# Kernel optimization log

Measured on AMD Instinct MI355X. Metric: run time of the kernel, lower is better.

The kernel has to match this reference:

```python
import jax, jax.numpy as jnp
import numpy as np

EPS = 1e-12


def _l2norm(x, axis):
    return x / jnp.maximum(jnp.linalg.norm(x, axis=axis, keepdims=True), EPS)


def _wn_weight(v, g):
    # weight norm over input axis (kernel_size=1): W = g * v / ||v||
    return g * v / jnp.maximum(jnp.linalg.norm(v, axis=0, keepdims=True), EPS)


def setup_inputs() -> dict:
    key = jax.random.key(0)
    ks = jax.random.split(key, 8)
    B, T, D = 16, 4096, 512
    N, K, d = 9, 1024, 8
    return {
        "z": jax.random.normal(ks[0], (B, T, D), dtype=jnp.float32),
        "in_v": jax.random.normal(ks[1], (N, D, d), dtype=jnp.float32) * 0.05,
        "in_g": jax.random.uniform(ks[2], (N, d), dtype=jnp.float32) + 0.5,
        "in_b": jax.random.normal(ks[3], (N, d), dtype=jnp.float32) * 0.01,
        "out_v": jax.random.normal(ks[4], (N, d, D), dtype=jnp.float32) * 0.05,
        "out_g": jax.random.uniform(ks[5], (N, D), dtype=jnp.float32) + 0.5,
        "out_b": jax.random.normal(ks[6], (N, D), dtype=jnp.float32) * 0.01,
        "codebooks": jax.random.normal(ks[7], (N, K, d), dtype=jnp.float32),
    }


def reference(z, in_v, in_g, in_b, out_v, out_g, out_b, codebooks):
    # Eval-mode ResidualVectorQuantize: n_quantizers = n_codebooks, mask all True.
    n_codebooks = codebooks.shape[0]
    residual = z
    z_q = jnp.zeros_like(z)
    commitment_loss = jnp.zeros((), z.dtype)
    codebook_loss = jnp.zeros((), z.dtype)
    codes, latents = [], []
    for i in range(n_codebooks):
        # in_proj (weight-normalized 1x1 conv == linear): [B,T,D] -> [B,T,d]
        W_in = _wn_weight(in_v[i], in_g[i])
        z_e = jnp.einsum("btd,dc->btc", residual, W_in) + in_b[i]
        # decode_latents: l2-normalize, pairwise sq-dist, nearest neighbor
        cb = codebooks[i]                      # [K, d] raw codebook
        enc_n = _l2norm(z_e, axis=-1)          # [B, T, d]
        cb_n = _l2norm(cb, axis=-1)            # [K, d]
        dist = (jnp.sum(enc_n * enc_n, -1, keepdims=True)
                - 2.0 * jnp.einsum("btc,kc->btk", enc_n, cb_n)
                + jnp.sum(cb_n * cb_n, -1))    # [B, T, K]
        indices = jnp.argmax(-dist, axis=-1)   # [B, T]
        z_q_i = cb[indices]                    # gather from raw codebook [B,T,d]
        # per-batch losses (mean over T, d)
        commit_i = jnp.mean((z_e - jax.lax.stop_gradient(z_q_i)) ** 2, axis=(1, 2))
        cbloss_i = jnp.mean((z_q_i - jax.lax.stop_gradient(z_e)) ** 2, axis=(1, 2))
        # straight-through estimator
        z_q_st = z_e + jax.lax.stop_gradient(z_q_i - z_e)
        # out_proj: [B,T,d] -> [B,T,D]
        W_out = _wn_weight(out_v[i], out_g[i])
        z_q_proj = jnp.einsum("btc,cd->btd", z_q_st, W_out) + out_b[i]
        z_q = z_q + z_q_proj
        residual = residual - z_q_proj
        commitment_loss = commitment_loss + commit_i.mean()
        codebook_loss = codebook_loss + cbloss_i.mean()
        codes.append(indices)
        latents.append(z_e)
    codes = jnp.stack(codes, axis=2)           # [B, T, N]
    latents = jnp.concatenate(latents, axis=2) # [B, T, N*d]
    return z_q, codes, latents, commitment_loss, codebook_loss
```

## Files before the change

kernel.cpp:

```cpp
#include <hip/hip_runtime.h>
#include <math.h>

#define ROWS   65536

#define WS_WPAD 0
#define WS_WOUT 49152
#define WS_CBT  86016
#define WS_SC   159744
#define WS_M    168960
#define WS_CACC 174144
#define WS_SOB  174216
#define WS_LOSS 174728

#define OUT_CODES 33554432
#define OUT_LAT   34144256
#define OUT_CLOSS 38862848
#define OUT_CBLOSS 38862849

#define SM_AST   0
#define SM_BS    4224
#define SM_P     0
#define SM_QLT   0
#define SM_REG2  9216
#define SM_CODES 18720
#define SM_WARR  19872

typedef float v2f __attribute__((ext_vector_type(2)));
__device__ __forceinline__ v2f fma2(v2f a, v2f b, v2f c){
    return __builtin_elementwise_fma(a, b, c);
}

__device__ __forceinline__ int pcol(int cc){ return (cc/9)*12 + (cc%9); }

__global__ __launch_bounds__(256) void prep1(const float* __restrict__ in_v,
    const float* __restrict__ in_g, const float* __restrict__ out_v,
    const float* __restrict__ out_g, const float* __restrict__ out_b,
    const float* __restrict__ cb, float* __restrict__ ws)
{
    int t = blockIdx.x*256 + threadIdx.x;
    if (t < 9216) {
        int i = t >> 10, k = t & 1023;
        const float* p = cb + (i*1024 + k)*8;
        float v[8]; float ssq = 0.f;
        #pragma unroll
        for (int c=0;c<8;c++){ v[c]=p[c]; ssq = fmaf(v[c],v[c],ssq); }
        float den = fmaxf(sqrtf(ssq), 1e-12f);
        float sc = 0.f;
        #pragma unroll
        for (int c=0;c<8;c++){ float cn = v[c]/den; ws[WS_CBT + (i*8+c)*1024 + k] = cn; sc = fmaf(cn,cn,sc); }
        ws[WS_SC + i*1024 + k] = sc;
    } else if (t < 13824) {
        int r = t - 9216; int j = r >> 9, tt = r & 511;
        float v[8]; float ssq = 0.f;
        #pragma unroll
        for (int a=0;a<8;a++){ v[a]=out_v[(j*8+a)*512+tt]; ssq=fmaf(v[a],v[a],ssq); }
        float den = fmaxf(sqrtf(ssq), 1e-12f);
        float g = out_g[j*512+tt];
        #pragma unroll
        for (int a=0;a<8;a++) ws[WS_WOUT + (j*8+a)*512 + tt] = g*v[a]/den;
    } else if (t < 18432) {
        int r = t - 13824;
        int w = r >> 6, l = r & 63;
        int i = w >> 3, c = w & 7;
        float v[8]; float ssq = 0.f;
        #pragma unroll
        for (int u=0;u<8;u++){ v[u] = in_v[(i*512 + l*8+u)*8 + c]; ssq = fmaf(v[u],v[u],ssq); }
        #pragma unroll
        for (int off=1; off<64; off<<=1) ssq += __shfl_xor(ssq, off, 64);
        float den = fmaxf(sqrtf(ssq), 1e-12f);
        float g = in_g[i*8+c];
        int pc = pcol(i*8+c);
        #pragma unroll
        for (int u=0;u<8;u++) ws[WS_WPAD + (l*8+u)*96 + pc] = g*v[u]/den;
    } else if (t < 18944) {
        int tt = t - 18432;
        float s = 0.f;
        for (int j=0;j<9;j++) s += out_b[j*512+tt];
        ws[WS_SOB + tt] = s;
    } else if (t == 18944) {
        *(double*)&ws[WS_LOSS] = 0.0;
    }
}

__global__ __launch_bounds__(256) void prep2(const float* __restrict__ out_b,
                                             float* __restrict__ ws)
{
    int g = blockIdx.x*256 + threadIdx.x;
    if (g < 41472) {
        int oi = g >> 3, part = g & 7;
        int j = oi / 576; int rem = oi % 576; int i = rem >> 6; int ab = rem & 63;
        int a = ab >> 3, b = ab & 7;
        int pc = pcol(i*8+b);
        const float* wo = ws + WS_WOUT + (j*8+a)*512 + part*64;
        const float* wp = ws + WS_WPAD + (part*64)*96 + pc;
        float s = 0.f;
        #pragma unroll
        for (int u=0; u<16; u++) {
            float4 w4 = *(const float4*)(wo + u*4);
            s = fmaf(w4.x, wp[(u*4+0)*96], s);
            s = fmaf(w4.y, wp[(u*4+1)*96], s);
            s = fmaf(w4.z, wp[(u*4+2)*96], s);
            s = fmaf(w4.w, wp[(u*4+3)*96], s);
        }
        #pragma unroll
        for (int off=1; off<8; off<<=1) s += __shfl_xor(s, off, 64);
        if (part == 0) ws[WS_M + oi] = s;
    } else if (g < 42048) {
        int r = g - 41472;
        int oi = r >> 3, part = r & 7;
        int i = oi >> 3, b = oi & 7;
        int pc = pcol(i*8+b);
        float s = 0.f;
        for (int u=0; u<64; u++) {
            int tt = part*64 + u;
            float bb = 0.f;
            for (int j=0;j<i;j++) bb += out_b[j*512+tt];
            s = fmaf(bb, ws[WS_WPAD + tt*96+pc], s);
        }
        #pragma unroll
        for (int off=1; off<8; off<<=1) s += __shfl_xor(s, off, 64);
        if (part == 0) ws[WS_CACC + oi] = s;
    }
}

__global__ __launch_bounds__(256, 2) void fused_all(
    const float* __restrict__ z, const float* __restrict__ in_b,
    const float* __restrict__ cbooks, float* __restrict__ ws, float* __restrict__ out)
{
    __shared__ __align__(16) float smem[19880];
    int tid = threadIdx.x;
    int brow = blockIdx.x * 128;

    {
        float* AsT = smem + SM_AST;
        float* Bs  = smem + SM_BS;
        int tr = tid & 31, tc = tid >> 5;
        v2f accp[4][4]; float acc8[4];
        #pragma unroll
        for (int r=0;r<4;r++){
            #pragma unroll
            for(int t2=0;t2<4;t2++) accp[r][t2] = (v2f){0.f,0.f};
            acc8[r]=0.f;
        }
        int kq = tid & 7, rr = tid >> 3;
        for (int kk=0; kk<16; kk++) {
            #pragma unroll
            for (int p=0;p<4;p++){
                int row = rr + p*32;
                float4 a = *(const float4*)(z + (size_t)(brow+row)*512 + kk*32 + kq*4);
                AsT[(kq     )*132 + row] = a.x;
                AsT[(kq +  8)*132 + row] = a.y;
                AsT[(kq + 16)*132 + row] = a.z;
                AsT[(kq + 24)*132 + row] = a.w;
            }
            #pragma unroll
            for (int p=0;p<3;p++){
                int idx = p*256 + tid;
                *(float4*)(Bs + idx*4) = *(const float4*)(ws + WS_WPAD + kk*32*96 + idx*4);
            }
            __syncthreads();
            #pragma unroll 4
            for (int k=0;k<32;k++){
                int sk = ((k&3)<<3) | (k>>2);
                float4 a  = *(const float4*)(AsT + sk*132 + tr*4);
                float4 b0 = *(const float4*)(Bs + k*96 + tc*12);
                float4 b1 = *(const float4*)(Bs + k*96 + tc*12 + 4);
                float  b8 = Bs[k*96 + tc*12 + 8];
                float av[4] = {a.x,a.y,a.z,a.w};
                v2f bp[4] = {{b0.x,b0.y},{b0.z,b0.w},{b1.x,b1.y},{b1.z,b1.w}};
                #pragma unroll
                for (int r=0;r<4;r++){
                    v2f ar = {av[r], av[r]};
                    #pragma unroll
                    for (int t2=0;t2<4;t2++) accp[r][t2] = fma2(ar, bp[t2], accp[r][t2]);
                    acc8[r] = fmaf(av[r], b8, acc8[r]);
                }
            }
            __syncthreads();
        }
        float* P = smem + SM_P;
        #pragma unroll
        for (int c=0;c<9;c++){
            int cc = tc*9+c;
            float bias = in_b[cc];
            #pragma unroll
            for (int r=0;r<4;r++){
                int rl = tr*4 + r;
                float val = (c<8) ? accp[r][c>>1][c&1] : acc8[r];
                P[rl*72 + cc] = val + bias;
            }
        }
        __syncthreads();
    }

    int w  = tid >> 6;
    int l  = tid & 63;
    int rowhalf = l >> 1;
    int ah = l & 1;
    int wrow = brow + w*32;
    int kb = l*16;
    float* P = smem + SM_P;
    float* zen_w = smem + SM_REG2 + w*384;
    float* codes_lds = smem + SM_CODES;

    float lacc = 0.f;
    v2f cbp[8][8];
    v2f hp[8];

    #pragma unroll 1
    for (int i=0; i<9; i++){
        const float* cbb = ws + WS_CBT + i*8192 + kb;
        #pragma unroll
        for (int c=0;c<8;c++){
            float4 A0 = *(const float4*)(cbb + c*1024);
            float4 A1 = *(const float4*)(cbb + c*1024 + 4);
            float4 A2 = *(const float4*)(cbb + c*1024 + 8);
            float4 A3 = *(const float4*)(cbb + c*1024 + 12);
            cbp[0][c] = (v2f){A0.x,A0.y}; cbp[1][c] = (v2f){A0.z,A0.w};
            cbp[2][c] = (v2f){A1.x,A1.y}; cbp[3][c] = (v2f){A1.z,A1.w};
            cbp[4][c] = (v2f){A2.x,A2.y}; cbp[5][c] = (v2f){A2.z,A2.w};
            cbp[6][c] = (v2f){A3.x,A3.y}; cbp[7][c] = (v2f){A3.z,A3.w};
        }
        {
            const float* scb = ws + WS_SC + i*1024 + kb;
            float4 s0 = *(const float4*)(scb);
            float4 s1 = *(const float4*)(scb + 4);
            float4 s2 = *(const float4*)(scb + 8);
            float4 s3 = *(const float4*)(scb + 12);
            hp[0] = (v2f){s0.x*-0.5f, s0.y*-0.5f}; hp[1] = (v2f){s0.z*-0.5f, s0.w*-0.5f};
            hp[2] = (v2f){s1.x*-0.5f, s1.y*-0.5f}; hp[3] = (v2f){s1.z*-0.5f, s1.w*-0.5f};
            hp[4] = (v2f){s2.x*-0.5f, s2.y*-0.5f}; hp[5] = (v2f){s2.z*-0.5f, s2.w*-0.5f};
            hp[6] = (v2f){s3.x*-0.5f, s3.y*-0.5f}; hp[7] = (v2f){s3.z*-0.5f, s3.w*-0.5f};
        }

        int row = wrow + rowhalf;
        int rib = w*32 + rowhalf;
        float* lat = out + OUT_LAT + (size_t)row*72 + i*8;
        float4 p0 = *(const float4*)(P + rib*72 + i*8);
        float4 p1 = *(const float4*)(P + rib*72 + i*8 + 4);
        v2f zep[4] = {{p0.x,p0.y},{p0.z,p0.w},{p1.x,p1.y},{p1.z,p1.w}};
        #pragma unroll
        for (int t2=0;t2<4;t2++){
            v2f cp = {ws[WS_CACC + i*8 + 2*t2], ws[WS_CACC + i*8 + 2*t2+1]};
            zep[t2] -= cp;
        }
        #pragma unroll 1
        for (int j=0;j<i;j++){
            int kj = (int)codes_lds[rib*9 + j];
            const float* qp = cbooks + (size_t)(j*1024+kj)*8;
            float4 q0 = *(const float4*)(qp);
            float4 q1 = *(const float4*)(qp+4);
            float qa[8] = {q0.x,q0.y,q0.z,q0.w,q1.x,q1.y,q1.z,q1.w};
            const float* M = ws + WS_M + (j*9+i)*64;
            #pragma unroll
            for (int a=0;a<8;a++){
                float4 m0 = *(const float4*)(M + a*8);
                float4 m1 = *(const float4*)(M + a*8 + 4);
                v2f nqa = {-qa[a], -qa[a]};
                zep[0] = fma2(nqa, (v2f){m0.x,m0.y}, zep[0]);
                zep[1] = fma2(nqa, (v2f){m0.z,m0.w}, zep[1]);
                zep[2] = fma2(nqa, (v2f){m1.x,m1.y}, zep[2]);
                zep[3] = fma2(nqa, (v2f){m1.z,m1.w}, zep[3]);
            }
        }
        float ssq = 0.f;
        #pragma unroll
        for (int c=0;c<8;c++){ float zc = zep[c>>1][c&1]; ssq = fmaf(zc,zc,ssq); }
        float den = fmaxf(sqrtf(ssq), 1e-12f);
        float rden = 1.0f/den;
        v2f rd2 = {rden, rden};
        v2f zenp[4];
        #pragma unroll
        for (int t2=0;t2<4;t2++) zenp[t2] = zep[t2]*rd2;
        if (ah == 0){
            float4 n0 = {zenp[0][0],zenp[0][1],zenp[1][0],zenp[1][1]};
            float4 n1 = {zenp[2][0],zenp[2][1],zenp[3][0],zenp[3][1]};
            *(float4*)(zen_w + rowhalf*12)     = n0;
            *(float4*)(zen_w + rowhalf*12 + 4) = n1;
        } else {
            float4 z0 = {zep[0][0],zep[0][1],zep[1][0],zep[1][1]};
            float4 z1 = {zep[2][0],zep[2][1],zep[3][0],zep[3][1]};
            *(float4*)(lat)   = z0;
            *(float4*)(lat+4) = z1;
        }

        int ksave = 0;
        #pragma unroll 2
        for (int rr=0; rr<32; rr++){
            float4 zv0 = *(const float4*)(zen_w + rr*12);
            float4 zv1 = *(const float4*)(zen_w + rr*12 + 4);
            float zr[8] = {zv0.x,zv0.y,zv0.z,zv0.w,zv1.x,zv1.y,zv1.z,zv1.w};
            v2f dp[8];
            #pragma unroll
            for (int p=0;p<8;p++) dp[p] = hp[p];
            #pragma unroll
            for (int c=0;c<8;c++){
                v2f zc = {zr[c], zr[c]};
                #pragma unroll
                for (int p=0;p<8;p++) dp[p] = fma2(zc, cbp[p][c], dp[p]);
            }
            float bv = -3.0e38f; int rel = 0;
            #pragma unroll
            for (int p=0;p<8;p++){
                float de = dp[p][0];
                bool ce = de > bv; rel = ce ? (2*p)   : rel; bv = ce ? de : bv;
                float dohalf = dp[p][1];
                bool co = dohalf > bv; rel = co ? (2*p+1) : rel; bv = co ? dohalf : bv;
            }
            int kfull = kb + rel;
            float wm = bv;
            #pragma unroll
            for (int off=1; off<64; off<<=1) wm = fmaxf(wm, __shfl_xor(wm, off, 64));
            unsigned long long msk = __ballot(bv == wm);
            int ln = __ffsll((long long)msk) - 1;
            int kwin = __shfl(kfull, ln, 64);
            ksave = (rowhalf == rr) ? kwin : ksave;
        }

        if (ah == 0){
            const float* qp = cbooks + (size_t)(i*1024+ksave)*8;
            float4 q0 = *(const float4*)(qp);
            float4 q1 = *(const float4*)(qp+4);
            float e0 = zep[0][0]-q0.x, e1 = zep[0][1]-q0.y, e2 = zep[1][0]-q0.z, e3 = zep[1][1]-q0.w;
            float e4 = zep[2][0]-q1.x, e5 = zep[2][1]-q1.y, e6 = zep[3][0]-q1.z, e7 = zep[3][1]-q1.w;
            lacc = fmaf(e0,e0,lacc); lacc = fmaf(e1,e1,lacc);
            lacc = fmaf(e2,e2,lacc); lacc = fmaf(e3,e3,lacc);
            lacc = fmaf(e4,e4,lacc); lacc = fmaf(e5,e5,lacc);
            lacc = fmaf(e6,e6,lacc); lacc = fmaf(e7,e7,lacc);
        } else {
            out[OUT_CODES + (size_t)row*9 + i] = (float)ksave;
            codes_lds[rib*9 + i] = (float)ksave;
        }
    }

    {
        float* warr = smem + SM_WARR;
        #pragma unroll
        for (int off=1; off<64; off<<=1) lacc += __shfl_xor(lacc, off, 64);
        if ((tid & 63)==0) warr[w] = lacc;
        __syncthreads();
        if (tid==0){
            double bs = (double)warr[0]+(double)warr[1]+(double)warr[2]+(double)warr[3];
            atomicAdd((double*)&ws[WS_LOSS], bs);
        }
    }

    __syncthreads();
    {
        float* QLT = smem + SM_QLT;
        float* Ws  = smem + SM_REG2;
        if (tid < 128){
            for (int j=0;j<9;j++){
                int kj = (int)codes_lds[tid*9 + j];
                const float* qp = cbooks + (size_t)(j*1024+kj)*8;
                float4 q0 = *(const float4*)qp;
                float4 q1 = *(const float4*)(qp+4);
                QLT[(j*8+0)*128 + tid] = q0.x;
                QLT[(j*8+1)*128 + tid] = q0.y;
                QLT[(j*8+2)*128 + tid] = q0.z;
                QLT[(j*8+3)*128 + tid] = q0.w;
                QLT[(j*8+4)*128 + tid] = q1.x;
                QLT[(j*8+5)*128 + tid] = q1.y;
                QLT[(j*8+6)*128 + tid] = q1.z;
                QLT[(j*8+7)*128 + tid] = q1.w;
            }
        }
        int tc = tid & 15, tr = tid >> 4;
        int aoff = tr*8;
        int boff = tc*8 + (tc>>3)*4;
        for (int cc=0; cc<4; cc++){
            __syncthreads();
            #pragma unroll
            for (int p=0;p<9;p++){
                int idx = p*256 + tid;
                int jr = idx >> 5; int cq = idx & 31;
                float4 wv = *(const float4*)(ws + WS_WOUT + jr*512 + cc*128 + cq*4);
                *(float4*)(Ws + jr*132 + cq*4 + (cq>>4)*4) = wv;
            }
            __syncthreads();
            v2f accp[8][4];
            #pragma unroll
            for (int r=0;r<8;r++){
                #pragma unroll
                for (int t2=0;t2<4;t2++) accp[r][t2] = (v2f){0.f,0.f};
            }
            #pragma unroll 2
            for (int k=0;k<72;k++){
                float4 a0 = *(const float4*)(QLT + k*128 + aoff);
                float4 a1 = *(const float4*)(QLT + k*128 + aoff + 4);
                float4 b0 = *(const float4*)(Ws + k*132 + boff);
                float4 b1 = *(const float4*)(Ws + k*132 + boff + 4);
                float av[8] = {a0.x,a0.y,a0.z,a0.w,a1.x,a1.y,a1.z,a1.w};
                v2f wp[4] = {{b0.x,b0.y},{b0.z,b0.w},{b1.x,b1.y},{b1.z,b1.w}};
                #pragma unroll
                for (int r=0;r<8;r++){
                    v2f ar = {av[r], av[r]};
                    #pragma unroll
                    for (int t2=0;t2<4;t2++) accp[r][t2] = fma2(ar, wp[t2], accp[r][t2]);
                }
            }
            float4 s0 = *(const float4*)(ws + WS_SOB + cc*128 + tc*8);
            float4 s1 = *(const float4*)(ws + WS_SOB + cc*128 + tc*8 + 4);
            #pragma unroll
            for (int r=0;r<8;r++){
                int row = brow + tr*8 + r;
                float4 o0 = {accp[r][0][0]+s0.x, accp[r][0][1]+s0.y, accp[r][1][0]+s0.z, accp[r][1][1]+s0.w};
                float4 o1 = {accp[r][2][0]+s1.x, accp[r][2][1]+s1.y, accp[r][3][0]+s1.z, accp[r][3][1]+s1.w};
                *(float4*)(out + (size_t)row*512 + cc*128 + tc*8)     = o0;
                *(float4*)(out + (size_t)row*512 + cc*128 + tc*8 + 4) = o1;
            }
        }
    }
}

__global__ void finalize(const float* __restrict__ ws, float* __restrict__ out)
{
    if (threadIdx.x == 0){
        double L = *(const double*)(ws + WS_LOSS);
        float lv = (float)(L * (1.0/524288.0));
        out[OUT_CLOSS]  = lv;
        out[OUT_CBLOSS] = lv;
    }
}

extern "C" void kernel_launch(void* const* d_in, const int* in_sizes, int n_in,
                              void* d_out, int out_size, void* d_ws, size_t ws_size,
                              hipStream_t stream) {
    const float* z     = (const float*)d_in[0];
    const float* in_v  = (const float*)d_in[1];
    const float* in_g  = (const float*)d_in[2];
    const float* in_b  = (const float*)d_in[3];
    const float* out_v = (const float*)d_in[4];
    const float* out_g = (const float*)d_in[5];
    const float* out_b = (const float*)d_in[6];
    const float* cb    = (const float*)d_in[7];
    float* out = (float*)d_out;
    float* ws  = (float*)d_ws;

    prep1<<<75, 256, 0, stream>>>(in_v, in_g, out_v, out_g, out_b, cb, ws);
    prep2<<<165, 256, 0, stream>>>(out_b, ws);
    fused_all<<<512, 256, 0, stream>>>(z, in_b, cb, ws, out);
    finalize<<<1, 64, 0, stream>>>(ws, out);
}
```

Baseline: 585.5 us.

## Stream codebook halves per row pair to cut register pressure in argmax loop

The codebook slice (8x16 values) and scaled norms are no longer held in registers for the whole 32-row scan. Each row pair now reloads two 8-column halves from global/L2 and evaluates both rows against them. The per-lane argmax uses a tree reduction, the two rows' wave reductions are interleaved, and the loss work is split across both lane halves. The aim is to lower VGPR use for better occupancy and more ILP, at the cost of repeated codebook loads inside the row loop.

```diff
diff --git a/kernel.cpp b/kernel.cpp
--- a/kernel.cpp
+++ b/kernel.cpp
@@ -204,35 +204,9 @@
     float* codes_lds = smem + SM_CODES;
 
     float lacc = 0.f;
-    v2f cbp[8][8];
-    v2f hp[8];
 
     #pragma unroll 1
     for (int i=0; i<9; i++){
-        const float* cbb = ws + WS_CBT + i*8192 + kb;
-        #pragma unroll
-        for (int c=0;c<8;c++){
-            float4 A0 = *(const float4*)(cbb + c*1024);
-            float4 A1 = *(const float4*)(cbb + c*1024 + 4);
-            float4 A2 = *(const float4*)(cbb + c*1024 + 8);
-            float4 A3 = *(const float4*)(cbb + c*1024 + 12);
-            cbp[0][c] = (v2f){A0.x,A0.y}; cbp[1][c] = (v2f){A0.z,A0.w};
-            cbp[2][c] = (v2f){A1.x,A1.y}; cbp[3][c] = (v2f){A1.z,A1.w};
-            cbp[4][c] = (v2f){A2.x,A2.y}; cbp[5][c] = (v2f){A2.z,A2.w};
-            cbp[6][c] = (v2f){A3.x,A3.y}; cbp[7][c] = (v2f){A3.z,A3.w};
-        }
-        {
-            const float* scb = ws + WS_SC + i*1024 + kb;
-            float4 s0 = *(const float4*)(scb);
-            float4 s1 = *(const float4*)(scb + 4);
-            float4 s2 = *(const float4*)(scb + 8);
-            float4 s3 = *(const float4*)(scb + 12);
-            hp[0] = (v2f){s0.x*-0.5f, s0.y*-0.5f}; hp[1] = (v2f){s0.z*-0.5f, s0.w*-0.5f};
-            hp[2] = (v2f){s1.x*-0.5f, s1.y*-0.5f}; hp[3] = (v2f){s1.z*-0.5f, s1.w*-0.5f};
-            hp[4] = (v2f){s2.x*-0.5f, s2.y*-0.5f}; hp[5] = (v2f){s2.z*-0.5f, s2.w*-0.5f};
-            hp[6] = (v2f){s3.x*-0.5f, s3.y*-0.5f}; hp[7] = (v2f){s3.z*-0.5f, s3.w*-0.5f};
-        }
-
         int row = wrow + rowhalf;
         int rib = w*32 + rowhalf;
         float* lat = out + OUT_LAT + (size_t)row*72 + i*8;
@@ -241,8 +215,8 @@
         v2f zep[4] = {{p0.x,p0.y},{p0.z,p0.w},{p1.x,p1.y},{p1.z,p1.w}};
         #pragma unroll
         for (int t2=0;t2<4;t2++){
-            v2f cp = {ws[WS_CACC + i*8 + 2*t2], ws[WS_CACC + i*8 + 2*t2+1]};
-            zep[t2] -= cp;
+            v2f cp2 = {ws[WS_CACC + i*8 + 2*t2], ws[WS_CACC + i*8 + 2*t2+1]};
+            zep[t2] -= cp2;
         }
         #pragma unroll 1
         for (int j=0;j<i;j++){
@@ -269,12 +243,10 @@
         float den = fmaxf(sqrtf(ssq), 1e-12f);
         float rden = 1.0f/den;
         v2f rd2 = {rden, rden};
-        v2f zenp[4];
-        #pragma unroll
-        for (int t2=0;t2<4;t2++) zenp[t2] = zep[t2]*rd2;
         if (ah == 0){
-            float4 n0 = {zenp[0][0],zenp[0][1],zenp[1][0],zenp[1][1]};
-            float4 n1 = {zenp[2][0],zenp[2][1],zenp[3][0],zenp[3][1]};
+            v2f zn0 = zep[0]*rd2, zn1 = zep[1]*rd2, zn2 = zep[2]*rd2, zn3 = zep[3]*rd2;
+            float4 n0 = {zn0[0],zn0[1],zn1[0],zn1[1]};
+            float4 n1 = {zn2[0],zn2[1],zn3[0],zn3[1]};
             *(float4*)(zen_w + rowhalf*12)     = n0;
             *(float4*)(zen_w + rowhalf*12 + 4) = n1;
         } else {
@@ -283,53 +255,108 @@
             *(float4*)(lat)   = z0;
             *(float4*)(lat+4) = z1;
         }
+        v2f zh0 = ah ? zep[2] : zep[0];
+        v2f zh1 = ah ? zep[3] : zep[1];
 
         int ksave = 0;
-        #pragma unroll 2
-        for (int rr=0; rr<32; rr++){
-            float4 zv0 = *(const float4*)(zen_w + rr*12);
-            float4 zv1 = *(const float4*)(zen_w + rr*12 + 4);
-            float zr[8] = {zv0.x,zv0.y,zv0.z,zv0.w,zv1.x,zv1.y,zv1.z,zv1.w};
-            v2f dp[8];
-            #pragma unroll
-            for (int p=0;p<8;p++) dp[p] = hp[p];
-            #pragma unroll
-            for (int c=0;c<8;c++){
-                v2f zc = {zr[c], zr[c]};
+        #pragma unroll 1
+        for (int rr=0; rr<32; rr+=2){
+            const float* zA = zen_w + rr*12;
+            const float* zB = zen_w + rr*12 + 12;
+            float bvA = -3.0e38f, bvB = -3.0e38f; int relA = 0, relB = 0;
+            #pragma unroll 1
+            for (int h=0; h<2; h++){
+                const float* cbb = ws + WS_CBT + i*8192 + kb + h*8;
+                v2f cp[4][8];
                 #pragma unroll
-                for (int p=0;p<8;p++) dp[p] = fma2(zc, cbp[p][c], dp[p]);
-            }
-            float bv = -3.0e38f; int rel = 0;
-            #pragma unroll
-            for (int p=0;p<8;p++){
-                float de = dp[p][0];
-                bool ce = de > bv; rel = ce ? (2*p)   : rel; bv = ce ? de : bv;
-                float dohalf = dp[p][1];
-                bool co = dohalf > bv; rel = co ? (2*p+1) : rel; bv = co ? dohalf : bv;
-            }
-            int kfull = kb + rel;
-            float wm = bv;
-            #pragma unroll
-            for (int off=1; off<64; off<<=1) wm = fmaxf(wm, __shfl_xor(wm, off, 64));
-            unsigned long long msk = __ballot(bv == wm);
-            int ln = __ffsll((long long)msk) - 1;
-            int kwin = __shfl(kfull, ln, 64);
-            ksave = (rowhalf == rr) ? kwin : ksave;
-        }
-
-        if (ah == 0){
-            const float* qp = cbooks + (size_t)(i*1024+ksave)*8;
-            float4 q0 = *(const float4*)(qp);
-            float4 q1 = *(const float4*)(qp+4);
-            float e0 = zep[0][0]-q0.x, e1 = zep[0][1]-q0.y, e2 = zep[1][0]-q0.z, e3 = zep[1][1]-q0.w;
-            float e4 = zep[2][0]-q1.x, e5 = zep[2][1]-q1.y, e6 = zep[3][0]-q1.z, e7 = zep[3][1]-q1.w;
+                for (int c=0;c<8;c++){
+                    float4 A0 = *(const float4*)(cbb + c*1024);
+                    float4 A1 = *(const float4*)(cbb + c*1024 + 4);
+                    cp[0][c]=(v2f){A0.x,A0.y}; cp[1][c]=(v2f){A0.z,A0.w};
+                    cp[2][c]=(v2f){A1.x,A1.y}; cp[3][c]=(v2f){A1.z,A1.w};
+                }
+                const float* scb = ws + WS_SC + i*1024 + kb + h*8;
+                float4 s0 = *(const float4*)(scb);
+                float4 s1 = *(const float4*)(scb+4);
+                v2f hh[4] = {{s0.x*-0.5f,s0.y*-0.5f},{s0.z*-0.5f,s0.w*-0.5f},
+                             {s1.x*-0.5f,s1.y*-0.5f},{s1.z*-0.5f,s1.w*-0.5f}};
+                {
+                    float4 zv0 = *(const float4*)(zA);
+                    float4 zv1 = *(const float4*)(zA+4);
+                    float zr[8] = {zv0.x,zv0.y,zv0.z,zv0.w,zv1.x,zv1.y,zv1.z,zv1.w};
+                    v2f d[4] = {hh[0],hh[1],hh[2],hh[3]};
+                    #pragma unroll
+                    for (int c=0;c<8;c++){
+                        v2f zc = {zr[c], zr[c]};
+                        #pragma unroll
+                        for (int p=0;p<4;p++) d[p] = fma2(zc, cp[p][c], d[p]);
+                    }
+                    bool t;
+                    float va = d[0][0]; int ia = 0;
+                    t = d[0][1] > va; va = t?d[0][1]:va; ia = t?1:ia;
+                    float vb = d[1][0]; int ib = 2;
+                    t = d[1][1] > vb; vb = t?d[1][1]:vb; ib = t?3:ib;
+                    float vc = d[2][0]; int ic = 4;
+                    t = d[2][1] > vc; vc = t?d[2][1]:vc; ic = t?5:ic;
+                    float vd = d[3][0]; int id_ = 6;
+                    t = d[3][1] > vd; vd = t?d[3][1]:vd; id_ = t?7:id_;
+                    t = vb > va; va = t?vb:va; ia = t?ib:ia;
+                    t = vd > vc; vc = t?vd:vc; ic = t?id_:ic;
+                    t = vc > va; va = t?vc:va; ia = t?ic:ia;
+                    t = va > bvA; bvA = t?va:bvA; relA = t?(h*8+ia):relA;
+                }
+                {
+                    float4 zv0 = *(const float4*)(zB);
+                    float4 zv1 = *(const float4*)(zB+4);
+                    float zr[8] = {zv0.x,zv0.y,zv0.z,zv0.w,zv1.x,zv1.y,zv1.z,zv1.w};
+                    v2f d[4] = {hh[0],hh[1],hh[2],hh[3]};
+                    #pragma unroll
+                    for (int c=0;c<8;c++){
+                        v2f zc = {zr[c], zr[c]};
+                        #pragma unroll
+                        for (int p=0;p<4;p++) d[p] = fma2(zc, cp[p][c], d[p]);
+                    }
+                    bool t;
+                    float va = d[0][0]; int ia = 0;
+                    t = d[0][1] > va; va = t?d[0][1]:va; ia = t?1:ia;
+                    float vb = d[1][0]; int ib = 2;
+                    t = d[1][1] > vb; vb = t?d[1][1]:vb; ib = t?3:ib;
+                    float vc = d[2][0]; int ic = 4;
+                    t = d[2][1] > vc; vc = t?d[2][1]:vc; ic = t?5:ic;
+                    float vd = d[3][0]; int id_ = 6;
+                    t = d[3][1] > vd; vd = t?d[3][1]:vd; id_ = t?7:id_;
+                    t = vb > va; va = t?vb:va; ia = t?ib:ia;
+                    t = vd > vc; vc = t?vd:vc; ic = t?id_:ic;
+                    t = vc > va; va = t?vc:va; ia = t?ic:ia;
+                    t = va > bvB; bvB = t?va:bvB; relB = t?(h*8+ia):relB;
+                }
+            }
+            float wmA = bvA, wmB = bvB;
+            #pragma unroll
+            for (int off=1; off<64; off<<=1){
+                wmA = fmaxf(wmA, __shfl_xor(wmA, off, 64));
+                wmB = fmaxf(wmB, __shfl_xor(wmB, off, 64));
+            }
+            unsigned long long mA = __ballot(bvA == wmA);
+            unsigned long long mB = __ballot(bvB == wmB);
+            int lnA = __ffsll((long long)mA) - 1;
+            int lnB = __ffsll((long long)mB) - 1;
+            int kA = __shfl(kb + relA, lnA, 64);
+            int kB = __shfl(kb + relB, lnB, 64);
+            ksave = (rowhalf == rr)   ? kA : ksave;
+            ksave = (rowhalf == rr+1) ? kB : ksave;
+        }
+
+        {
+            const float* qp = cbooks + (size_t)(i*1024+ksave)*8 + ah*4;
+            float4 q = *(const float4*)(qp);
+            float e0 = zh0[0]-q.x, e1 = zh0[1]-q.y, e2 = zh1[0]-q.z, e3 = zh1[1]-q.w;
             lacc = fmaf(e0,e0,lacc); lacc = fmaf(e1,e1,lacc);
             lacc = fmaf(e2,e2,lacc); lacc = fmaf(e3,e3,lacc);
-            lacc = fmaf(e4,e4,lacc); lacc = fmaf(e5,e5,lacc);
-            lacc = fmaf(e6,e6,lacc); lacc = fmaf(e7,e7,lacc);
-        } else {
-            out[OUT_CODES + (size_t)row*9 + i] = (float)ksave;
-            codes_lds[rib*9 + i] = (float)ksave;
+            if (ah){
+                out[OUT_CODES + (size_t)row*9 + i] = (float)ksave;
+                codes_lds[rib*9 + i] = (float)ksave;
+            }
         }
     }
 
```

After: 974.8 us. +66.5%, slower.
